# Kernel optimization log

Measured on AMD Instinct MI355X. Metric: run time of the kernel, lower is better.

## Reference

```python
import jax, jax.numpy as jnp
import numpy as np

D_MODEL = 2048
N_HEADS = 32
N_KV = 8
HEAD_DIM = D_MODEL // N_HEADS  # 64
D_FF = 8192
ROPE_BASE = 10000.0
EPS = 1e-5
B, S = 2, 2048


def setup_inputs() -> dict:
    key = jax.random.key(0)
    ks = jax.random.split(key, 8)
    s = 0.02
    qkv_out = (N_HEADS + 2 * N_KV) * HEAD_DIM
    return {
        "x": jax.random.normal(ks[0], (B, S, D_MODEL), jnp.float32),
        "w_norm1": jnp.ones((D_MODEL,), jnp.float32),
        "w_qkv": jax.random.normal(ks[1], (D_MODEL, qkv_out), jnp.float32) * s,
        "w_out": jax.random.normal(ks[2], (D_MODEL, D_MODEL), jnp.float32) * s,
        "w_norm2": jnp.ones((D_MODEL,), jnp.float32),
        "w_gate": jax.random.normal(ks[3], (D_MODEL, D_FF), jnp.float32) * s,
        "w_up": jax.random.normal(ks[4], (D_MODEL, D_FF), jnp.float32) * s,
        "w_down": jax.random.normal(ks[5], (D_FF, D_MODEL), jnp.float32) * s,
    }


def _rmsnorm(x, w):
    var = jnp.mean(x * x, axis=-1, keepdims=True)
    return x * jax.lax.rsqrt(var + EPS) * w


def _rope(x, cos, sin):
    # x: [b, s, h, d]; cos/sin: [s, d/2]; non-interleaved (NeoX half split)
    half = x.shape[-1] // 2
    x1, x2 = x[..., :half], x[..., half:]
    c = cos[None, :, None, :]
    sn = sin[None, :, None, :]
    return jnp.concatenate([x1 * c - x2 * sn, x1 * sn + x2 * c], axis=-1)


def _forward(x, w_norm1, w_qkv, w_out, w_norm2, w_gate, w_up, w_down):
    b, s, d = x.shape
    # --- attention block ---
    h = _rmsnorm(x, w_norm1)
    qkv = h @ w_qkv  # [b, s, (H + 2*KV) * hd]
    q = qkv[..., : N_HEADS * HEAD_DIM].reshape(b, s, N_HEADS, HEAD_DIM)
    kv = qkv[..., N_HEADS * HEAD_DIM:].reshape(b, s, 2, N_KV, HEAD_DIM)
    k, v = kv[:, :, 0], kv[:, :, 1]

    inv_freq = 1.0 / (ROPE_BASE ** (jnp.arange(0, HEAD_DIM, 2, dtype=jnp.float32) / HEAD_DIM))
    t = jnp.arange(s, dtype=jnp.float32)
    freqs = t[:, None] * inv_freq[None, :]  # [s, hd/2]
    cos, sin = jnp.cos(freqs), jnp.sin(freqs)
    q = _rope(q, cos, sin)
    k = _rope(k, cos, sin)

    # GQA: repeat_interleave kv heads to match q heads
    g = N_HEADS // N_KV
    k = jnp.repeat(k, g, axis=2)  # [b, s, H, hd]
    v = jnp.repeat(v, g, axis=2)

    scale = 1.0 / np.sqrt(HEAD_DIM)
    scores = jnp.einsum("bqhd,bkhd->bhqk", q, k) * scale
    causal = jnp.tril(jnp.ones((s, s), bool))
    scores = jnp.where(causal[None, None], scores, jnp.finfo(scores.dtype).min)
    attn = jax.nn.softmax(scores, axis=-1)
    ctx = jnp.einsum("bhqk,bkhd->bqhd", attn, v).reshape(b, s, N_HEADS * HEAD_DIM)
    x = x + ctx @ w_out

    # --- MLP block (SwiGLU) ---
    h2 = _rmsnorm(x, w_norm2)
    mlp = (jax.nn.silu(h2 @ w_gate) * (h2 @ w_up)) @ w_down
    return x + mlp


def reference(x, w_norm1, w_qkv, w_out, w_norm2, w_gate, w_up, w_down):
    return _forward(x, w_norm1, w_qkv, w_out, w_norm2, w_gate, w_up, w_down)
```

## Files before the change

kernel.cpp:

```cpp
#include <hip/hip_runtime.h>
#include <stdint.h>

#define D_MODEL 2048
#define S_LEN   2048
#define NTOK    4096
#define QKV_N   3072
#define DFF     8192

typedef float  f32x4   __attribute__((ext_vector_type(4)));
typedef float  f32x16  __attribute__((ext_vector_type(16)));
typedef __bf16 bf16x8  __attribute__((ext_vector_type(8)));
typedef unsigned short u16;
typedef unsigned short u16x8 __attribute__((ext_vector_type(8)));

__device__ __forceinline__ float b2f(u16 u){ union{float f; uint32_t i;} v; v.i = ((uint32_t)u) << 16; return v.f; }
__device__ __forceinline__ u16 f2b(float f){
  union{float f; uint32_t i;} v; v.f = f;
  uint32_t r = v.i + 0x7FFFu + ((v.i >> 16) & 1u);
  return (u16)(r >> 16);
}

__device__ __forceinline__ void gload_lds16(const void* gsrc, void* ldst){
  __builtin_amdgcn_global_load_lds(
      (const __attribute__((address_space(1))) void*)gsrc,
      (__attribute__((address_space(3))) void*)ldst,
      16, 0, 0);
}

__device__ __forceinline__ void conv_tiles(const float* W, const float* W2, u16* WT,
    int Nfull, int Kt, int Nt, int k0g, int n0g, int rmul, void* ldsbuf)
{
  if (W == nullptr) return;
  float* tf = (float*)ldsbuf;
  const int tt  = threadIdx.x;
  const int nTn = Nt >> 6;
  const int nT  = (Kt >> 6) * nTn;
  const int bid = (blockIdx.z * gridDim.y + blockIdx.y) * gridDim.x + blockIdx.x;
  const int gsz = gridDim.x * gridDim.y * gridDim.z;
  const int c4 = (tt & 15) << 2;
  const int r  = tt >> 4;
  for (int tile = bid; tile < nT; tile += gsz) {
    const int k0 = (tile / nTn) << 6, n0 = (tile % nTn) << 6;
    for (int m = 0; m < 2; ++m) {
      const float* Ws = m ? W2 : W;
      if (m && W2 == nullptr) break;
      __syncthreads();
      if (tt < 256) {
#pragma unroll
        for (int i = 0; i < 4; ++i) {
          int row = r + i * 16;
          float4 v = *reinterpret_cast<const float4*>(&Ws[(size_t)(k0g + k0 + row) * Nfull + n0g + n0 + c4]);
          tf[row * 65 + c4 + 0] = v.x; tf[row * 65 + c4 + 1] = v.y;
          tf[row * 65 + c4 + 2] = v.z; tf[row * 65 + c4 + 3] = v.w;
        }
      }
      __syncthreads();
      if (tt < 256) {
#pragma unroll
        for (int i = 0; i < 4; ++i) {
          int n = r + i * 16;
          ushort4 ov;
          ov.x = f2b(tf[(c4 + 0) * 65 + n]); ov.y = f2b(tf[(c4 + 1) * 65 + n]);
          ov.z = f2b(tf[(c4 + 2) * 65 + n]); ov.w = f2b(tf[(c4 + 3) * 65 + n]);
          *reinterpret_cast<ushort4*>(&WT[(size_t)((n0 + n) * rmul + m) * Kt + k0 + c4]) = ov;
        }
      }
    }
  }
}

__global__ void sincos_kernel(float* __restrict__ ct, float* __restrict__ st)
{
  int idx = blockIdx.x * 256 + threadIdx.x;
  if (idx >= S_LEN * 32) return;
  int p = idx >> 5, i = idx & 31;
  double freq = pow(10000.0, -((double)(2*i)) / 64.0);
  double ang  = (double)p * freq;
  ct[idx] = (float)cos(ang);
  st[idx] = (float)sin(ang);
}

template<bool BF16IN>
__global__ __launch_bounds__(256) void rmsnorm_kernel(const void* __restrict__ xin, const float* __restrict__ w, u16* __restrict__ out,
                                                      const float* cvW, const float* cvW2, u16* cvWT, int cvNfull, int cvKt, int cvNt, int cvK0g, int cvN0g, int cvRm)
{
  __shared__ float tfbuf[64 * 65];
  const int row = blockIdx.x;
  const int t = threadIdx.x;
  float v[8];
  if (BF16IN) {
    const u16* xr = ((const u16*)xin) + (size_t)row * D_MODEL;
    u16x8 a = *reinterpret_cast<const u16x8*>(&xr[t*8]);
#pragma unroll
    for (int j = 0; j < 8; ++j) v[j] = b2f(a[j]);
  } else {
    const float* xr = ((const float*)xin) + (size_t)row * D_MODEL;
    float4 a = *reinterpret_cast<const float4*>(&xr[t*8]);
    float4 c = *reinterpret_cast<const float4*>(&xr[t*8+4]);
    v[0]=a.x; v[1]=a.y; v[2]=a.z; v[3]=a.w; v[4]=c.x; v[5]=c.y; v[6]=c.z; v[7]=c.w;
  }
  float ss = 0.f;
#pragma unroll
  for (int j = 0; j < 8; ++j) ss += v[j]*v[j];
#pragma unroll
  for (int d = 1; d < 64; d <<= 1) ss += __shfl_xor(ss, d);
  __shared__ float red[4];
  if ((t & 63) == 0) red[t >> 6] = ss;
  __syncthreads();
  ss = red[0] + red[1] + red[2] + red[3];
  const float sc = rsqrtf(ss * (1.0f / (float)D_MODEL) + 1e-5f);
  float4 w0 = *reinterpret_cast<const float4*>(&w[t*8]);
  float4 w1 = *reinterpret_cast<const float4*>(&w[t*8+4]);
  u16x8 o;
  o[0]=f2b(v[0]*sc*w0.x); o[1]=f2b(v[1]*sc*w0.y); o[2]=f2b(v[2]*sc*w0.z); o[3]=f2b(v[3]*sc*w0.w);
  o[4]=f2b(v[4]*sc*w1.x); o[5]=f2b(v[5]*sc*w1.y); o[6]=f2b(v[6]*sc*w1.z); o[7]=f2b(v[7]*sc*w1.w);
  *reinterpret_cast<u16x8*>(&out[(size_t)row * D_MODEL + t*8]) = o;
  conv_tiles(cvW, cvW2, cvWT, cvNfull, cvKt, cvNt, cvK0g, cvN0g, cvRm, tfbuf);
}

template<int EPI>
__device__ __forceinline__ void epi_store(size_t idx, float v, float* Cf, u16* Cb,
                                          const float* resf, const u16* resb, const u16* other)
{
  if (EPI == 2)      Cb[idx] = f2b(v / (1.0f + __expf(-v)));
  else if (EPI == 3) Cb[idx] = f2b(v * b2f(other[idx]));
  else if (EPI == 4) Cb[idx] = f2b(v);
  else if (EPI == 5) Cf[idx] += v;
  else if (EPI == 6) Cb[idx] = f2b(v + resf[idx]);
  else if (EPI == 7) Cf[idx] = v + b2f(resb[idx]);
  else if (EPI == 9) {
    float pv = __shfl_xor(v, 1);
    float gate = (threadIdx.x & 1) ? pv : v;
    float up   = (threadIdx.x & 1) ? v  : pv;
    if (!(threadIdx.x & 1)) Cb[idx] = f2b(gate / (1.0f + __expf(-gate)) * up);
  }
}

template<int EPI>
__global__ __launch_bounds__(512, 2) void gemm8p_kernel(
    const u16* __restrict__ A, const u16* __restrict__ BT, const u16* __restrict__ BT2,
    int K, int lda, int ldb, int ldc, int n_off,
    float* Cf, u16* Cb,
    const float* __restrict__ resf, const u16* __restrict__ resb, const u16* other,
    const float* cvW, const float* cvW2, u16* cvWT, int cvNfull, int cvKt, int cvNt, int cvK0g, int cvN0g, int cvRm)
{
  __shared__ u16 lds[65536];
  const int tid = threadIdx.x;
  const int w = tid >> 6, lane = tid & 63;
  const int g = lane >> 4, lr = lane & 15;
  const int wm = w >> 2, wn = w & 3;
  int fid = blockIdx.y * gridDim.x + blockIdx.x;
  const int nwg = gridDim.x * gridDim.y;
  fid = (fid & 7) * (nwg >> 3) + (fid >> 3);
  const int bn = fid / gridDim.y, bm = fid % gridDim.y;
  const int NT = K >> 6;
  const int NI = NT >> 1;

  const int srow = tid >> 3;
  const int sg   = (tid & 7) ^ (srow & 7);
  const u16* Asrc = A + (size_t)(bm * 256) * lda;
  const u16* Bsrc;
  if (EPI == 9) Bsrc = (bn < 16) ? BT + (size_t)(bn * 256) * ldb
                                 : BT2 + (size_t)(bn * 256 - 4096) * ldb;
  else          Bsrc = BT + (size_t)(bn * 256) * ldb;

  const int agc0 = ((0 + g) ^ (lr & 7)) * 8;
  const int agc1 = ((4 + g) ^ (lr & 7)) * 8;

  f32x4 acc[8][4];
#pragma unroll
  for (int i = 0; i < 8; ++i)
#pragma unroll
    for (int j = 0; j < 4; ++j) acc[i][j] = (f32x4){0.f, 0.f, 0.f, 0.f};
  bf16x8 af[4][2], bf0[2][2], bf1[2][2];

#define STAGE_H(isB, h, b, T) do {                                           \
    int tc = ((T) < NT) ? (T) : (NT - 1);                                    \
    const u16* sb = (isB) ? Bsrc : Asrc;                                     \
    const int  sld = (isB) ? ldb : lda;                                      \
    const u16* s0 = sb + (size_t)((h)*128 + srow) * sld + tc*64 + sg*8;      \
    u16* dst = &lds[(b)*32768 + (isB)*16384 + (h)*8192 + tid*8];             \
    gload_lds16(s0, dst);                                                    \
    gload_lds16(s0 + (size_t)64 * sld, dst + 4096);                          \
  } while (0)

#define LOADA(mih, b) { _Pragma("unroll") for (int q = 0; q < 4; ++q) {      \
    const u16* rp = &lds[(b)*32768 + (wm*128 + (mih)*64 + q*16 + lr) * 64];  \
    af[q][0] = *(const bf16x8*)(rp + agc0);                                  \
    af[q][1] = *(const bf16x8*)(rp + agc1); } }

#define LOADB(dst, nih, b) { _Pragma("unroll") for (int nq = 0; nq < 2; ++nq) { \
    const u16* rp = &lds[(b)*32768 + 16384 + (wn*64 + (nih)*32 + nq*16 + lr) * 64]; \
    dst[nq][0] = *(const bf16x8*)(rp + agc0);                                \
    dst[nq][1] = *(const bf16x8*)(rp + agc1); } }

#define MM(mih, nih, BF) {                                                   \
    __builtin_amdgcn_s_setprio(1);                                           \
    _Pragma("unroll") for (int kk = 0; kk < 2; ++kk)                         \
      _Pragma("unroll") for (int q = 0; q < 4; ++q)                          \
        _Pragma("unroll") for (int nq = 0; nq < 2; ++nq)                     \
          acc[(mih)*4+q][(nih)*2+nq] = __builtin_amdgcn_mfma_f32_16x16x32_bf16( \
              af[q][kk], BF[nq][kk], acc[(mih)*4+q][(nih)*2+nq], 0, 0, 0);   \
    __builtin_amdgcn_s_setprio(0); }

#define SYNC_MID  __builtin_amdgcn_s_barrier();                              \
                  asm volatile("s_waitcnt lgkmcnt(0)" ::: "memory");         \
                  __builtin_amdgcn_sched_barrier(0);
#define PHEND     __builtin_amdgcn_s_barrier();
#define PHEND_VM  asm volatile("s_waitcnt vmcnt(4)" ::: "memory");           \
                  __builtin_amdgcn_s_barrier();

  STAGE_H(0, 0, 0, 0); STAGE_H(0, 1, 0, 0);
  STAGE_H(1, 0, 0, 0); STAGE_H(1, 1, 0, 0);
  STAGE_H(1, 0, 1, 1); STAGE_H(1, 1, 1, 1);
  asm volatile("s_waitcnt vmcnt(4)" ::: "memory");
  __builtin_amdgcn_s_barrier();

  for (int i = 0; i < NI; ++i) {
    const int t0 = 2 * i;
    LOADA(0, 0); LOADB(bf0, 0, 0);
    STAGE_H(0, 0, 1, t0 + 1);
    SYNC_MID; MM(0, 0, bf0); PHEND;
    LOADB(bf1, 1, 0);
    STAGE_H(0, 1, 1, t0 + 1);
    SYNC_MID; MM(0, 1, bf1); PHEND;
    LOADA(1, 0);
    STAGE_H(1, 0, 0, t0 + 2);
    SYNC_MID; MM(1, 1, bf1); PHEND;
    STAGE_H(1, 1, 0, t0 + 2);
    SYNC_MID; MM(1, 0, bf0); PHEND_VM;
    LOADA(0, 1); LOADB(bf0, 0, 1);
    STAGE_H(0, 0, 0, t0 + 2);
    SYNC_MID; MM(0, 0, bf0); PHEND;
    LOADB(bf1, 1, 1);
    STAGE_H(0, 1, 0, t0 + 2);
    SYNC_MID; MM(0, 1, bf1); PHEND;
    LOADA(1, 1);
    STAGE_H(1, 0, 1, t0 + 3);
    SYNC_MID; MM(1, 1, bf1); PHEND;
    STAGE_H(1, 1, 1, t0 + 3);
    SYNC_MID; MM(1, 0, bf0); PHEND_VM;
  }
#undef STAGE_H
#undef LOADA
#undef LOADB
#undef MM

#pragma unroll
  for (int mi = 0; mi < 8; ++mi) {
    const int rowOff = (mi >> 2) * 64 + (mi & 3) * 16;
#pragma unroll
    for (int ni = 0; ni < 4; ++ni) {
      const int colOff = (ni >> 1) * 32 + (ni & 1) * 16;
#pragma unroll
      for (int j = 0; j < 4; ++j) {
        int row = bm*256 + wm*128 + rowOff + g*4 + j;
        int col = n_off + bn*256 + wn*64 + colOff + lr;
        size_t idx = (EPI == 9) ? ((size_t)row * ldc + (col >> 1))
                                : ((size_t)row * ldc + col);
        epi_store<EPI>(idx, acc[mi][ni][j], Cf, Cb, resf, resb, other);
      }
    }
  }
  conv_tiles(cvW, cvW2, cvWT, cvNfull, cvKt, cvNt, cvK0g, cvN0g, cvRm, lds);
}

template<int EPI>
__global__ __launch_bounds__(512) void gemm128_kernel(
    const u16* __restrict__ A, const u16* __restrict__ BT,
    int K, int lda, int ldb, int ldc, int n_off,
    float* Cf, u16* Cb,
    const float* __restrict__ resf, const u16* __restrict__ resb, const u16* other,
    const float* c1W, const float* c1W2, u16* c1WT, int c1Nfull, int c1Kt, int c1Nt, int c1K0g, int c1N0g, int c1Rm,
    const float* c2W, const float* c2W2, u16* c2WT, int c2Nfull, int c2Kt, int c2Nt, int c2K0g, int c2N0g, int c2Rm)
{
  __shared__ u16 lds[49152];
  const int tid = threadIdx.x;
  const int w = tid >> 6, lane = tid & 63;
  const int g = lane >> 4, lr = lane & 15;
  const int wm = w >> 2, wn = w & 3;
  int fid = blockIdx.y * gridDim.x + blockIdx.x;
  const int nwg = gridDim.x * gridDim.y;
  fid = (fid & 7) * (nwg >> 3) + (fid >> 3);
  const int bn = fid / gridDim.y, bm = fid % gridDim.y;
  const int NT = K >> 6;
  const int NI = NT >> 1;

  const int srow = tid >> 3;
  const int sg   = (tid & 7) ^ (srow & 7);
  const u16* Asrc = A  + (size_t)(bm * 128) * lda;
  const u16* Bsrc = BT + (size_t)(bn * 256) * ldb;

  const int agc0 = ((0 + g) ^ (lr & 7)) * 8;
  const int agc1 = ((4 + g) ^ (lr & 7)) * 8;

  f32x4 acc[4][4];
#pragma unroll
  for (int i = 0; i < 4; ++i)
#pragma unroll
    for (int j = 0; j < 4; ++j) acc[i][j] = (f32x4){0.f, 0.f, 0.f, 0.f};
  bf16x8 af[2][2], bf0[2][2], bf1[2][2];

#define STAGE_A(b, T) do {                                                   \
    int tc = ((T) < NT) ? (T) : (NT - 1);                                    \
    const u16* s0 = Asrc + (size_t)srow * lda + tc*64 + sg*8;                \
    u16* dst = &lds[(b)*24576 + tid*8];                                      \
    gload_lds16(s0, dst);                                                    \
    gload_lds16(s0 + (size_t)64 * lda, dst + 4096);                          \
  } while (0)

#define STAGE_BH(h, b, T) do {                                               \
    int tc = ((T) < NT) ? (T) : (NT - 1);                                    \
    const u16* s0 = Bsrc + (size_t)((h)*128 + srow) * ldb + tc*64 + sg*8;    \
    u16* dst = &lds[(b)*24576 + 8192 + (h)*8192 + tid*8];                    \
    gload_lds16(s0, dst);                                                    \
    gload_lds16(s0 + (size_t)64 * ldb, dst + 4096);                         \
  } while (0)

#define LOADA(mih, b) { _Pragma("unroll") for (int q = 0; q < 2; ++q) {      \
    const u16* rp = &lds[(b)*24576 + (wm*64 + (mih)*32 + q*16 + lr) * 64];   \
    af[q][0] = *(const bf16x8*)(rp + agc0);                                  \
    af[q][1] = *(const bf16x8*)(rp + agc1); } }

#define LOADB(dst, nih, b) { _Pragma("unroll") for (int nq = 0; nq < 2; ++nq) { \
    const u16* rp = &lds[(b)*24576 + 8192 + (wn*64 + (nih)*32 + nq*16 + lr) * 64]; \
    dst[nq][0] = *(const bf16x8*)(rp + agc0);                                \
    dst[nq][1] = *(const bf16x8*)(rp + agc1); } }

#define MM(mih, nih, BF) {                                                   \
    __builtin_amdgcn_s_setprio(1);                                           \
    _Pragma("unroll") for (int kk = 0; kk < 2; ++kk)                         \
      _Pragma("unroll") for (int q = 0; q < 2; ++q)                          \
        _Pragma("unroll") for (int nq = 0; nq < 2; ++nq)                     \
          acc[(mih)*2+q][(nih)*2+nq] = __builtin_amdgcn_mfma_f32_16x16x32_bf16( \
              af[q][kk], BF[nq][kk], acc[(mih)*2+q][(nih)*2+nq], 0, 0, 0);   \
    __builtin_amdgcn_s_setprio(0); }

  STAGE_A(0, 0); STAGE_BH(0, 0, 0); STAGE_BH(1, 0, 0);
  STAGE_BH(0, 1, 1); STAGE_BH(1, 1, 1);
  asm volatile("s_waitcnt vmcnt(4)" ::: "memory");
  __builtin_amdgcn_s_barrier();

  for (int i = 0; i < NI; ++i) {
    const int t0 = 2 * i;
    LOADA(0, 0); LOADB(bf0, 0, 0);
    STAGE_A(1, t0 + 1);
    SYNC_MID; MM(0, 0, bf0); PHEND;
    LOADB(bf1, 1, 0);
    STAGE_BH(0, 0, t0 + 2);
    SYNC_MID; MM(0, 1, bf1); PHEND;
    LOADA(1, 0);
    STAGE_BH(1, 0, t0 + 2);
    SYNC_MID; MM(1, 1, bf1); PHEND;
    STAGE_A(0, t0 + 2);
    SYNC_MID; MM(1, 0, bf0);
    asm volatile("s_waitcnt vmcnt(6)" ::: "memory");
    __builtin_amdgcn_s_barrier();
    LOADA(0, 1); LOADB(bf0, 0, 1);
    SYNC_MID; MM(0, 0, bf0); PHEND;
    LOADB(bf1, 1, 1);
    STAGE_BH(0, 1, t0 + 3);
    SYNC_MID; MM(0, 1, bf1); PHEND;
    LOADA(1, 1);
    STAGE_BH(1, 1, t0 + 3);
    SYNC_MID; MM(1, 1, bf1); PHEND;
    SYNC_MID; MM(1, 0, bf0);
    asm volatile("s_waitcnt vmcnt(4)" ::: "memory");
    __builtin_amdgcn_s_barrier();
  }
#undef STAGE_A
#undef STAGE_BH
#undef LOADA
#undef LOADB
#undef MM
#undef SYNC_MID
#undef PHEND
#undef PHEND_VM

#pragma unroll
  for (int mi = 0; mi < 4; ++mi) {
    const int rowOff = (mi >> 1) * 32 + (mi & 1) * 16;
#pragma unroll
    for (int ni = 0; ni < 4; ++ni) {
      const int colOff = (ni >> 1) * 32 + (ni & 1) * 16;
#pragma unroll
      for (int j = 0; j < 4; ++j) {
        int row = bm*128 + wm*64 + rowOff + g*4 + j;
        int col = n_off + bn*256 + wn*64 + colOff + lr;
        epi_store<EPI>((size_t)row * ldc + col, acc[mi][ni][j], Cf, Cb, resf, resb, other);
      }
    }
  }
  conv_tiles(c1W, c1W2, c1WT, c1Nfull, c1Kt, c1Nt, c1K0g, c1N0g, c1Rm, lds);
  conv_tiles(c2W, c2W2, c2WT, c2Nfull, c2Kt, c2Nt, c2K0g, c2N0g, c2Rm, lds);
}

__global__ __launch_bounds__(256) void rope_kernel(
    const u16* __restrict__ qkv, const float* __restrict__ ct, const float* __restrict__ st,
    u16* __restrict__ Kt, u16* __restrict__ VT)
{
  const int tok = blockIdx.x;
  const int b = tok >> 11, s = tok & (S_LEN - 1);
  const int w = threadIdx.x >> 6, lane = threadIdx.x & 63;
  const size_t base = (size_t)tok * QKV_N;
  for (int slot = w; slot < 16; slot += 4) {
    int col = (slot < 8) ? 2048 + slot * 64 : 2560 + (slot - 8) * 64;
    float v = b2f(qkv[base + col + lane]);
    if (slot < 8) {
      int i = lane & 31;
      float c = ct[s * 32 + i], sn = st[s * 32 + i];
      float p = b2f(qkv[base + col + (lane ^ 32)]);
      v = (lane < 32) ? (v * c - p * sn) : (v * c + p * sn);
    }
    u16 ob = f2b(v);
    if (slot < 8) Kt[((size_t)(b * 8 + slot)     * S_LEN + s) * 64 + lane] = ob;
    else          VT[((size_t)(b * 8 + slot - 8) * 64 + lane) * S_LEN + s] = ob;
  }
}

#define ASCALE 0.1803368801111204f
__global__ __launch_bounds__(256, 2) void attn_kernel(
    const u16* __restrict__ qkv, const u16* __restrict__ Kt,
    const u16* __restrict__ VT, u16* __restrict__ ctx,
    const float* __restrict__ ct, const float* __restrict__ st,
    const float* cvW, const float* cvW2, u16* cvWT, int cvNfull, int cvKt, int cvNt, int cvK0g, int cvN0g, int cvRm)
{
  __shared__ float tfbuf[64 * 65];
  const int fid = blockIdx.y * gridDim.x + blockIdx.x;
  const int idx = fid >> 3;
  const int bh  = (fid & 7) * 8 + (idx & 7);
  const int y   = idx >> 3;
  const int wid = threadIdx.x >> 6;
  const int lane = threadIdx.x & 63;
  const int b = bh >> 5, h = bh & 31;
  const int kvh = (b << 3) + (h >> 2);
  const int jj = y * 4 + wid;
  const int cq = lane & 31;
  const int hi = lane >> 5;

  const u16* Kp = Kt + (size_t)kvh * S_LEN * 64 + cq * 64 + hi * 8;
  const u16* Vbase = VT + (size_t)kvh * 64 * S_LEN + hi * 8;
  const u16* Vp[4];
#pragma unroll
  for (int v = 0; v < 4; ++v)
    Vp[v] = Vbase + (size_t)((v & 1) * 32 + cq) * S_LEN + (v >> 1) * 16;

  __shared__ float xch[4][32];

#define ATT_LOADK(KF, T) { _Pragma("unroll") for (int q_ = 0; q_ < 4; ++q_) \
    KF[q_] = *(const bf16x8*)(Kp + (T) * 2048 + q_ * 16); }
#define ATT_LOADV(VF, T) { _Pragma("unroll") for (int v_ = 0; v_ < 4; ++v_) \
    VF[v_] = *(const bf16x8*)(Vp[v_] + (T) * 32); }

#define ATT_QK(S, KF) do {                                                   \
    S = (f32x16){};                                                          \
    S = __builtin_amdgcn_mfma_f32_32x32x16_bf16(KF[0], qf[0], S, 0, 0, 0);   \
    S = __builtin_amdgcn_mfma_f32_32x32x16_bf16(KF[1], qf[1], S, 0, 0, 0);   \
    S = __builtin_amdgcn_mfma_f32_32x32x16_bf16(KF[2], qf[2], S, 0, 0, 0);   \
    S = __builtin_amdgcn_mfma_f32_32x32x16_bf16(KF[3], qf[3], S, 0, 0, 0);   \
  } while (0)

#define ATT_FIN(S, VF, T) do {                                               \
    float p[16];                                                             \
    _Pragma("unroll") for (int r = 0; r < 16; ++r) p[r] = S[r];              \
    if ((T) == nt - 1) {                                                     \
      _Pragma("unroll") for (int r = 0; r < 16; ++r) {                       \
        int kk = (r & 3) + 8 * (r >> 2) + 4 * hi;                            \
        if (kk > cq) p[r] = -1e30f;                                          \
      }                                                                      \
    }                                                                        \
    float m0_ = fmaxf(fmaxf(p[0], p[1]), p[2]);                              \
    float m1_ = fmaxf(fmaxf(p[3], p[4]), p[5]);                              \
    float m2_ = fmaxf(fmaxf(p[6], p[7]), p[8]);                              \
    float m3_ = fmaxf(fmaxf(p[9], p[10]), p[11]);                            \
    float m4_ = fmaxf(fmaxf(p[12], p[13]), p[14]);                           \
    float tmax = fmaxf(fmaxf(fmaxf(m0_, m1_), m2_), fmaxf(fmaxf(m3_, m4_), p[15])); \
    tmax = fmaxf(tmax, __shfl_xor(tmax, 32));                                \
    if (!__all(tmax <= m + 8.0f)) {                                          \
      float mn = fmaxf(m, tmax);                                             \
      float corr = exp2f(m - mn);                                            \
      m = mn;                                                                \
      l *= corr;                                                             \
      if (hi == 0) xch[wid][cq] = corr;                                      \
      asm volatile("s_waitcnt lgkmcnt(0)" ::: "memory");                     \
      __builtin_amdgcn_sched_barrier(0);                                     \
      float4 c0 = *reinterpret_cast<const float4*>(&xch[wid][4 * hi + 0]);   \
      float4 c1 = *reinterpret_cast<const float4*>(&xch[wid][4 * hi + 8]);   \
      float4 c2 = *reinterpret_cast<const float4*>(&xch[wid][4 * hi + 16]);  \
      float4 c3 = *reinterpret_cast<const float4*>(&xch[wid][4 * hi + 24]);  \
      float ca[16] = {c0.x,c0.y,c0.z,c0.w, c1.x,c1.y,c1.z,c1.w,              \
                      c2.x,c2.y,c2.z,c2.w, c3.x,c3.y,c3.z,c3.w};             \
      _Pragma("unroll") for (int r = 0; r < 16; ++r) { o0[r] *= ca[r]; o1[r] *= ca[r]; } \
    }                                                                        \
    _Pragma("unroll") for (int r = 0; r < 16; ++r) p[r] = exp2f(p[r] - m);   \
    {                                                                        \
      float a0 = p[0]+p[1], a1 = p[2]+p[3], a2 = p[4]+p[5], a3 = p[6]+p[7];  \
      float a4 = p[8]+p[9], a5 = p[10]+p[11], a6 = p[12]+p[13], a7 = p[14]+p[15]; \
      float b0_ = a0+a1, b1_ = a2+a3, b2_ = a4+a5, b3_ = a6+a7;              \
      l += (b0_+b1_) + (b2_+b3_);                                            \
    }                                                                        \
    uint32_t wds[8], pw[8];                                                  \
    _Pragma("unroll") for (int j = 0; j < 8; ++j) {                          \
      uint32_t wv;                                                           \
      asm("v_cvt_pk_bf16_f32 %0, %1, %2" : "=v"(wv) : "v"(p[2*j]), "v"(p[2*j+1])); \
      wds[j] = wv;                                                           \
    }                                                                        \
    _Pragma("unroll") for (int j = 0; j < 8; ++j) pw[j] = __shfl_xor(wds[j], 32); \
    union { uint32_t u[4]; bf16x8 v; } pa0, pa1;                             \
    pa0.u[0] = hi ? pw[2]  : wds[0];                                         \
    pa0.u[1] = hi ? pw[3]  : wds[1];                                         \
    pa0.u[2] = hi ? wds[2] : pw[0];                                          \
    pa0.u[3] = hi ? wds[3] : pw[1];                                          \
    pa1.u[0] = hi ? pw[6]  : wds[4];                                         \
    pa1.u[1] = hi ? pw[7]  : wds[5];                                         \
    pa1.u[2] = hi ? wds[6] : pw[4];                                          \
    pa1.u[3] = hi ? wds[7] : pw[5];                                          \
    o0 = __builtin_amdgcn_mfma_f32_32x32x16_bf16(pa0.v, VF[0], o0, 0, 0, 0); \
    o0 = __builtin_amdgcn_mfma_f32_32x32x16_bf16(pa1.v, VF[2], o0, 0, 0, 0); \
    o1 = __builtin_amdgcn_mfma_f32_32x32x16_bf16(pa0.v, VF[1], o1, 0, 0, 0); \
    o1 = __builtin_amdgcn_mfma_f32_32x32x16_bf16(pa1.v, VF[3], o1, 0, 0, 0); \
  } while (0)

#pragma unroll 1
  for (int task = 0; task < 2; ++task) {
    const int qt = task ? (63 - jj) : jj;
    const int q0 = qt << 5;
    const int nt = qt + 1;

    bf16x8 qf[4];
    {
      const u16* Qr = qkv + (size_t)(b * S_LEN + q0 + cq) * QKV_N + h * 64 + hi * 8;
      u16 qr[4][8];
#pragma unroll
      for (int t = 0; t < 4; ++t)
        *reinterpret_cast<u16x8*>(qr[t]) = *reinterpret_cast<const u16x8*>(Qr + t * 16);
      const float* cb = ct + (size_t)(q0 + cq) * 32 + hi * 8;
      const float* sb = st + (size_t)(q0 + cq) * 32 + hi * 8;
      union { u16 u[8]; bf16x8 v; } qo[4];
#pragma unroll
      for (int t = 0; t < 2; ++t) {
        float4 c0 = *reinterpret_cast<const float4*>(cb + 16 * t);
        float4 c1 = *reinterpret_cast<const float4*>(cb + 16 * t + 4);
        float4 s0 = *reinterpret_cast<const float4*>(sb + 16 * t);
        float4 s1 = *reinterpret_cast<const float4*>(sb + 16 * t + 4);
        float cc[8] = {c0.x,c0.y,c0.z,c0.w, c1.x,c1.y,c1.z,c1.w};
        float ssn[8] = {s0.x,s0.y,s0.z,s0.w, s1.x,s1.y,s1.z,s1.w};
#pragma unroll
        for (int i = 0; i < 8; ++i) {
          float lo = b2f(qr[t][i]), hif = b2f(qr[t + 2][i]);
          qo[t].u[i]     = f2b((lo * cc[i] - hif * ssn[i]) * ASCALE);
          qo[t + 2].u[i] = f2b((hif * cc[i] + lo * ssn[i]) * ASCALE);
        }
      }
#pragma unroll
      for (int t = 0; t < 4; ++t) qf[t] = qo[t].v;
    }

    f32x16 o0 = {}, o1 = {};
    float m = -1e30f, l = 0.f;

    bf16x8 kfE[4], kfO[4], vfE[4], vfO[4];
    f32x16 sE, sO;
    ATT_LOADK(kfE, 0); ATT_LOADV(vfE, 0);
    if (nt > 1) ATT_LOADK(kfO, 1);
    ATT_QK(sE, kfE);

    for (int t = 0; t < nt; ) {
      if (t + 2 < nt) ATT_LOADK(kfE, t + 2);
      if (t + 1 < nt) { ATT_LOADV(vfO, t + 1); ATT_QK(sO, kfO); }
      ATT_FIN(sE, vfE, t);
      ++t; if (t >= nt) break;
      if (t + 2 < nt) ATT_LOADK(kfO, t + 2);
      if (t + 1 < nt) { ATT_LOADV(vfE, t + 1); ATT_QK(sE, kfE); }
      ATT_FIN(sO, vfO, t);
      ++t;
    }

    l += __shfl_xor(l, 32);
    float linv = 1.0f / l;
    if (hi == 0) xch[wid][cq] = linv;
    asm volatile("s_waitcnt lgkmcnt(0)" ::: "memory");
    __builtin_amdgcn_sched_barrier(0);
    float4 n0 = *reinterpret_cast<const float4*>(&xch[wid][4 * hi + 0]);
    float4 n1 = *reinterpret_cast<const float4*>(&xch[wid][4 * hi + 8]);
    float4 n2 = *reinterpret_cast<const float4*>(&xch[wid][4 * hi + 16]);
    float4 n3 = *reinterpret_cast<const float4*>(&xch[wid][4 * hi + 24]);
    float na[16] = {n0.x,n0.y,n0.z,n0.w, n1.x,n1.y,n1.z,n1.w,
                    n2.x,n2.y,n2.z,n2.w, n3.x,n3.y,n3.z,n3.w};
#pragma unroll
    for (int r = 0; r < 16; ++r) {
      int row = (r & 3) + 8 * (r >> 2) + 4 * hi;
      size_t base = (size_t)(b * S_LEN + q0 + row) * D_MODEL + h * 64;
      ctx[base + cq]      = f2b(o0[r] * na[r]);
      ctx[base + 32 + cq] = f2b(o1[r] * na[r]);
    }
  }
#undef ATT_LOADK
#undef ATT_LOADV
#undef ATT_QK
#undef ATT_FIN

  conv_tiles(cvW, cvW2, cvWT, cvNfull, cvKt, cvNt, cvK0g, cvN0g, cvRm, tfbuf);
}

#define NOCV nullptr, nullptr, nullptr, 0, 0, 0, 0, 0, 1
extern "C" void kernel_launch(void* const* d_in, const int* in_sizes, int n_in,
                              void* d_out, int out_size, void* d_ws, size_t ws_size,
                              hipStream_t stream)
{
  const float* x     = (const float*)d_in[0];
  const float* wn1   = (const float*)d_in[1];
  const float* wqkv  = (const float*)d_in[2];
  const float* wout  = (const float*)d_in[3];
  const float* wn2   = (const float*)d_in[4];
  const float* wgate = (const float*)d_in[5];
  const float* wup   = (const float*)d_in[6];
  const float* wdown = (const float*)d_in[7];
  float* out = (float*)d_out;
  char* ws = (char*)d_ws;

  float* cosT = (float*)(ws + 0);
  float* sinT = (float*)(ws + 262144);
  u16*   U1   = (u16*)  (ws + 524288);
  u16*   U2   = (u16*)  (ws + 17301504);
  u16*   x1b  = (u16*)  (ws + 34078720);
  char*  S    = ws + 50855936;
  u16*   hB   = (u16*)(S + 0);
  u16*   qkvB = (u16*)(S + 16777216);
  u16*   kB   = (u16*)(S + 41943040);
  u16*   vtB  = (u16*)(S + 46137344);
  u16*   ctxB = (u16*)(S + 0);
  u16*   h2B  = (u16*)(S + 0);
  u16*   slab = (u16*)(S + 16777216);
  u16*   U7   = (u16*)(S + 50331648);

  sincos_kernel<<<dim3(256), 256, 0, stream>>>(cosT, sinT);
  rmsnorm_kernel<false><<<dim3(NTOK), 256, 0, stream>>>(x, wn1, hB,
      wqkv, nullptr, U1, 3072, 2048, 3072, 0, 0, 1);

  gemm128_kernel<4><<<dim3(12, 32), 512, 0, stream>>>(hB, U1, 2048, 2048, 2048, 3072, 0,
      nullptr, qkvB, nullptr, nullptr, nullptr,
      wout, nullptr, U7, 2048, 2048, 2048, 0, 0, 1, NOCV);
  rope_kernel<<<dim3(NTOK), 256, 0, stream>>>(qkvB, cosT, sinT, kB, vtB);
  attn_kernel<<<dim3(64, 8), 256, 0, stream>>>(qkvB, kB, vtB, ctxB, cosT, sinT,
      wgate, wup, U1, 8192, 2048, 2048, 0, 0, 2);

  gemm128_kernel<6><<<dim3(8, 32), 512, 0, stream>>>(ctxB, U7, 2048, 2048, 2048, 2048, 0,
      nullptr, x1b, x, nullptr, nullptr,
      wgate, wup, U2, 8192, 2048, 2048, 0, 2048, 2, NOCV);

  rmsnorm_kernel<true><<<dim3(NTOK), 256, 0, stream>>>(x1b, wn2, h2B,
      wdown, nullptr, U7, 2048, 4096, 2048, 0, 0, 1);

  gemm8p_kernel<9><<<dim3(32, 16), 512, 0, stream>>>(h2B, U1, U2, 2048, 2048, 2048, 4096, 0,
      nullptr, slab, nullptr, nullptr, nullptr, NOCV);
  gemm128_kernel<7><<<dim3(8, 32), 512, 0, stream>>>(slab, U7, 4096, 4096, 4096, 2048, 0,
      out, nullptr, nullptr, x1b, nullptr,
      wgate, wup, U1, 8192, 2048, 2048, 0, 4096, 2,
      wgate, wup, U2, 8192, 2048, 2048, 0, 6144, 2);
  gemm8p_kernel<9><<<dim3(32, 16), 512, 0, stream>>>(h2B, U1, U2, 2048, 2048, 2048, 4096, 0,
      nullptr, slab, nullptr, nullptr, nullptr,
      wdown, nullptr, U7, 2048, 4096, 2048, 4096, 0, 1);
  gemm128_kernel<5><<<dim3(8, 32), 512, 0, stream>>>(slab, U7, 4096, 4096, 4096, 2048, 0,
      out, nullptr, nullptr, nullptr, nullptr, NOCV, NOCV);
}
```

Before: 776.8 us.

## Process attention KV tiles in pairs with joint max and single rescale

Restructures the attention inner loop to load and compute two 32-key tiles at once, computing one combined row max and doing at most one online-softmax rescale per pair instead of per tile. An odd final tile is handled by a single-tile path. This halves the cross-lane max reduction and rescale checks, but drops the software prefetch pipeline: loads for a pair are now issued right before use, which may expose memory latency and raises register pressure. It also adds SYNC_MID/PHEND macro definitions in the GEMM section.

```diff
diff --git a/kernel.cpp b/kernel.cpp
--- a/kernel.cpp
+++ b/kernel.cpp
@@ -335,6 +335,11 @@
           acc[(mih)*2+q][(nih)*2+nq] = __builtin_amdgcn_mfma_f32_16x16x32_bf16( \
               af[q][kk], BF[nq][kk], acc[(mih)*2+q][(nih)*2+nq], 0, 0, 0);   \
     __builtin_amdgcn_s_setprio(0); }
+
+#define SYNC_MID  __builtin_amdgcn_s_barrier();                              \
+                  asm volatile("s_waitcnt lgkmcnt(0)" ::: "memory");         \
+                  __builtin_amdgcn_sched_barrier(0);
+#define PHEND     __builtin_amdgcn_s_barrier();
 
   STAGE_A(0, 0); STAGE_BH(0, 0, 0); STAGE_BH(1, 0, 0);
   STAGE_BH(0, 1, 1); STAGE_BH(1, 1, 1);
@@ -375,7 +380,6 @@
 #undef MM
 #undef SYNC_MID
 #undef PHEND
-#undef PHEND_VM
 
 #pragma unroll
   for (int mi = 0; mi < 4; ++mi) {
@@ -460,24 +464,9 @@
     S = __builtin_amdgcn_mfma_f32_32x32x16_bf16(KF[3], qf[3], S, 0, 0, 0);   \
   } while (0)
 
-#define ATT_FIN(S, VF, T) do {                                               \
-    float p[16];                                                             \
-    _Pragma("unroll") for (int r = 0; r < 16; ++r) p[r] = S[r];              \
-    if ((T) == nt - 1) {                                                     \
-      _Pragma("unroll") for (int r = 0; r < 16; ++r) {                       \
-        int kk = (r & 3) + 8 * (r >> 2) + 4 * hi;                            \
-        if (kk > cq) p[r] = -1e30f;                                          \
-      }                                                                      \
-    }                                                                        \
-    float m0_ = fmaxf(fmaxf(p[0], p[1]), p[2]);                              \
-    float m1_ = fmaxf(fmaxf(p[3], p[4]), p[5]);                              \
-    float m2_ = fmaxf(fmaxf(p[6], p[7]), p[8]);                              \
-    float m3_ = fmaxf(fmaxf(p[9], p[10]), p[11]);                            \
-    float m4_ = fmaxf(fmaxf(p[12], p[13]), p[14]);                           \
-    float tmax = fmaxf(fmaxf(fmaxf(m0_, m1_), m2_), fmaxf(fmaxf(m3_, m4_), p[15])); \
-    tmax = fmaxf(tmax, __shfl_xor(tmax, 32));                                \
-    if (!__all(tmax <= m + 8.0f)) {                                          \
-      float mn = fmaxf(m, tmax);                                             \
+#define ATT_RESCALE(TMAX) do {                                               \
+    if (!__all((TMAX) <= m + 8.0f)) {                                        \
+      float mn = fmaxf(m, (TMAX));                                           \
       float corr = exp2f(m - mn);                                            \
       m = mn;                                                                \
       l *= corr;                                                             \
@@ -492,33 +481,85 @@
                       c2.x,c2.y,c2.z,c2.w, c3.x,c3.y,c3.z,c3.w};             \
       _Pragma("unroll") for (int r = 0; r < 16; ++r) { o0[r] *= ca[r]; o1[r] *= ca[r]; } \
     }                                                                        \
-    _Pragma("unroll") for (int r = 0; r < 16; ++r) p[r] = exp2f(p[r] - m);   \
-    {                                                                        \
-      float a0 = p[0]+p[1], a1 = p[2]+p[3], a2 = p[4]+p[5], a3 = p[6]+p[7];  \
-      float a4 = p[8]+p[9], a5 = p[10]+p[11], a6 = p[12]+p[13], a7 = p[14]+p[15]; \
-      float b0_ = a0+a1, b1_ = a2+a3, b2_ = a4+a5, b3_ = a6+a7;              \
-      l += (b0_+b1_) + (b2_+b3_);                                            \
-    }                                                                        \
+  } while (0)
+
+#define ATT_PACK(P, PA0, PA1) do {                                           \
     uint32_t wds[8], pw[8];                                                  \
     _Pragma("unroll") for (int j = 0; j < 8; ++j) {                          \
       uint32_t wv;                                                           \
-      asm("v_cvt_pk_bf16_f32 %0, %1, %2" : "=v"(wv) : "v"(p[2*j]), "v"(p[2*j+1])); \
+      asm("v_cvt_pk_bf16_f32 %0, %1, %2" : "=v"(wv) : "v"((P)[2*j]), "v"((P)[2*j+1])); \
       wds[j] = wv;                                                           \
     }                                                                        \
     _Pragma("unroll") for (int j = 0; j < 8; ++j) pw[j] = __shfl_xor(wds[j], 32); \
+    PA0.u[0] = hi ? pw[2]  : wds[0];                                         \
+    PA0.u[1] = hi ? pw[3]  : wds[1];                                         \
+    PA0.u[2] = hi ? wds[2] : pw[0];                                          \
+    PA0.u[3] = hi ? wds[3] : pw[1];                                          \
+    PA1.u[0] = hi ? pw[6]  : wds[4];                                         \
+    PA1.u[1] = hi ? pw[7]  : wds[5];                                         \
+    PA1.u[2] = hi ? wds[6] : pw[4];                                          \
+    PA1.u[3] = hi ? wds[7] : pw[5];                                          \
+  } while (0)
+
+#define ATT_FIN1(S, VF) do {                                                 \
+    float p[16];                                                             \
+    _Pragma("unroll") for (int r = 0; r < 16; ++r) p[r] = S[r];              \
+    _Pragma("unroll") for (int r = 0; r < 16; ++r) {                         \
+      int kk = (r & 3) + 8 * (r >> 2) + 4 * hi;                              \
+      if (kk > cq) p[r] = -1e30f;                                            \
+    }                                                                        \
+    float m0_ = fmaxf(fmaxf(p[0], p[1]), p[2]);                              \
+    float m1_ = fmaxf(fmaxf(p[3], p[4]), p[5]);                              \
+    float m2_ = fmaxf(fmaxf(p[6], p[7]), p[8]);                              \
+    float m3_ = fmaxf(fmaxf(p[9], p[10]), p[11]);                            \
+    float m4_ = fmaxf(fmaxf(p[12], p[13]), p[14]);                           \
+    float tmax = fmaxf(fmaxf(fmaxf(m0_, m1_), m2_), fmaxf(fmaxf(m3_, m4_), p[15])); \
+    tmax = fmaxf(tmax, __shfl_xor(tmax, 32));                                \
+    ATT_RESCALE(tmax);                                                       \
+    float ts_ = 0.f;                                                         \
+    _Pragma("unroll") for (int r = 0; r < 16; ++r) { p[r] = exp2f(p[r] - m); ts_ += p[r]; } \
+    l += ts_;                                                                \
     union { uint32_t u[4]; bf16x8 v; } pa0, pa1;                             \
-    pa0.u[0] = hi ? pw[2]  : wds[0];                                         \
-    pa0.u[1] = hi ? pw[3]  : wds[1];                                         \
-    pa0.u[2] = hi ? wds[2] : pw[0];                                          \
-    pa0.u[3] = hi ? wds[3] : pw[1];                                          \
-    pa1.u[0] = hi ? pw[6]  : wds[4];                                         \
-    pa1.u[1] = hi ? pw[7]  : wds[5];                                         \
-    pa1.u[2] = hi ? wds[6] : pw[4];                                          \
-    pa1.u[3] = hi ? wds[7] : pw[5];                                          \
+    ATT_PACK(p, pa0, pa1);                                                   \
     o0 = __builtin_amdgcn_mfma_f32_32x32x16_bf16(pa0.v, VF[0], o0, 0, 0, 0); \
     o0 = __builtin_amdgcn_mfma_f32_32x32x16_bf16(pa1.v, VF[2], o0, 0, 0, 0); \
     o1 = __builtin_amdgcn_mfma_f32_32x32x16_bf16(pa0.v, VF[1], o1, 0, 0, 0); \
     o1 = __builtin_amdgcn_mfma_f32_32x32x16_bf16(pa1.v, VF[3], o1, 0, 0, 0); \
+  } while (0)
+
+#define ATT_FIN2(SA, SB, VFA, VFB, MASKB) do {                               \
+    float p[32];                                                             \
+    _Pragma("unroll") for (int r = 0; r < 16; ++r) { p[r] = SA[r]; p[16+r] = SB[r]; } \
+    if (MASKB) {                                                             \
+      _Pragma("unroll") for (int r = 0; r < 16; ++r) {                       \
+        int kk = (r & 3) + 8 * (r >> 2) + 4 * hi;                            \
+        if (kk > cq) p[16+r] = -1e30f;                                       \
+      }                                                                      \
+    }                                                                        \
+    float mx[8];                                                             \
+    _Pragma("unroll") for (int j = 0; j < 8; ++j)                            \
+      mx[j] = fmaxf(fmaxf(p[4*j], p[4*j+1]), fmaxf(p[4*j+2], p[4*j+3]));     \
+    float tmax = fmaxf(fmaxf(fmaxf(mx[0], mx[1]), fmaxf(mx[2], mx[3])),      \
+                       fmaxf(fmaxf(mx[4], mx[5]), fmaxf(mx[6], mx[7])));     \
+    tmax = fmaxf(tmax, __shfl_xor(tmax, 32));                                \
+    ATT_RESCALE(tmax);                                                       \
+    _Pragma("unroll") for (int r = 0; r < 32; ++r) p[r] = exp2f(p[r] - m);   \
+    {                                                                        \
+      float s1_ = 0.f, s2_ = 0.f;                                            \
+      _Pragma("unroll") for (int r = 0; r < 16; ++r) { s1_ += p[r]; s2_ += p[16+r]; } \
+      l += s1_ + s2_;                                                        \
+    }                                                                        \
+    union { uint32_t u[4]; bf16x8 v; } pa0, pa1, pb0, pb1;                   \
+    ATT_PACK(p, pa0, pa1);                                                   \
+    ATT_PACK((p + 16), pb0, pb1);                                            \
+    o0 = __builtin_amdgcn_mfma_f32_32x32x16_bf16(pa0.v, VFA[0], o0, 0, 0, 0); \
+    o0 = __builtin_amdgcn_mfma_f32_32x32x16_bf16(pa1.v, VFA[2], o0, 0, 0, 0); \
+    o1 = __builtin_amdgcn_mfma_f32_32x32x16_bf16(pa0.v, VFA[1], o1, 0, 0, 0); \
+    o1 = __builtin_amdgcn_mfma_f32_32x32x16_bf16(pa1.v, VFA[3], o1, 0, 0, 0); \
+    o0 = __builtin_amdgcn_mfma_f32_32x32x16_bf16(pb0.v, VFB[0], o0, 0, 0, 0); \
+    o0 = __builtin_amdgcn_mfma_f32_32x32x16_bf16(pb1.v, VFB[2], o0, 0, 0, 0); \
+    o1 = __builtin_amdgcn_mfma_f32_32x32x16_bf16(pb0.v, VFB[1], o1, 0, 0, 0); \
+    o1 = __builtin_amdgcn_mfma_f32_32x32x16_bf16(pb1.v, VFB[3], o1, 0, 0, 0); \
   } while (0)
 
 #pragma unroll 1
@@ -559,21 +600,24 @@
     f32x16 o0 = {}, o1 = {};
     float m = -1e30f, l = 0.f;
 
-    bf16x8 kfE[4], kfO[4], vfE[4], vfO[4];
-    f32x16 sE, sO;
-    ATT_LOADK(kfE, 0); ATT_LOADV(vfE, 0);
-    if (nt > 1) ATT_LOADK(kfO, 1);
-    ATT_QK(sE, kfE);
-
-    for (int t = 0; t < nt; ) {
-      if (t + 2 < nt) ATT_LOADK(kfE, t + 2);
-      if (t + 1 < nt) { ATT_LOADV(vfO, t + 1); ATT_QK(sO, kfO); }
-      ATT_FIN(sE, vfE, t);
-      ++t; if (t >= nt) break;
-      if (t + 2 < nt) ATT_LOADK(kfO, t + 2);
-      if (t + 1 < nt) { ATT_LOADV(vfE, t + 1); ATT_QK(sE, kfE); }
-      ATT_FIN(sO, vfO, t);
-      ++t;
+    const int npair = nt >> 1;
+    bf16x8 kfA[4], kfB[4], vfA[4], vfB[4];
+
+#pragma unroll 1
+    for (int i = 0; i < npair; ++i) {
+      const int Ta = 2 * i, Tb = 2 * i + 1;
+      ATT_LOADK(kfA, Ta); ATT_LOADK(kfB, Tb);
+      ATT_LOADV(vfA, Ta); ATT_LOADV(vfB, Tb);
+      f32x16 sA, sB;
+      ATT_QK(sA, kfA); ATT_QK(sB, kfB);
+      ATT_FIN2(sA, sB, vfA, vfB, (Tb == nt - 1));
+    }
+    if (nt & 1) {
+      const int T = nt - 1;
+      ATT_LOADK(kfA, T); ATT_LOADV(vfA, T);
+      f32x16 sA;
+      ATT_QK(sA, kfA);
+      ATT_FIN1(sA, vfA);
     }
 
     l += __shfl_xor(l, 32);
@@ -598,7 +642,10 @@
 #undef ATT_LOADK
 #undef ATT_LOADV
 #undef ATT_QK
-#undef ATT_FIN
+#undef ATT_RESCALE
+#undef ATT_PACK
+#undef ATT_FIN1
+#undef ATT_FIN2
 
   conv_tiles(cvW, cvW2, cvWT, cvNfull, cvKt, cvNt, cvK0g, cvN0g, cvRm, tfbuf);
 }
```

Measured after the change: 775.1 us. About the same (-0.2%).
